# Kernel optimization log

Measured on AMD Instinct MI355X. Metric: run time of the kernel, lower is better.

## Reference

```python
import jax, jax.numpy as jnp
import numpy as np

B, T, C, DU, OUT = 16, 2048, 1024, 1024, 512
CIF_THRESHOLD = 1.0


def setup_inputs():
    key = jax.random.key(0)
    k0, k1, k2, k3, k4, k5 = jax.random.split(key, 6)
    encoder_out = jax.random.normal(k0, (B, T, C), dtype=jnp.float32)
    input_lengths = (T // 2 + jax.random.randint(k1, (B,), 0, T // 2)).astype(jnp.int32)
    target_lengths = (200 + jax.random.randint(k2, (B,), 0, 300)).astype(jnp.int32)
    s = 1.0 / np.sqrt(C)
    Wd = jax.random.uniform(k3, (DU, C), jnp.float32, -s, s)
    bd = jnp.zeros((DU,), jnp.float32)
    sp = 1.0 / np.sqrt(DU)
    Wp = jax.random.uniform(k4, (1, DU), jnp.float32, -sp, sp)
    bp = jnp.zeros((1,), jnp.float32)
    Wo = jax.random.uniform(k5, (OUT, C), jnp.float32, -s, s)
    return {"encoder_out": encoder_out, "input_lengths": input_lengths,
            "target_lengths": target_lengths, "Wd": Wd, "bd": bd,
            "Wp": Wp, "bp": bp, "Wo": Wo}


def _cif_forward(encoder_out, input_lengths, target_lengths, Wd, bd, Wp, bp, Wo):
    Bsz, Tlen, Cdim = encoder_out.shape
    pos = jnp.arange(Tlen)
    not_pad = (pos[None, :] < input_lengths[:, None]).astype(encoder_out.dtype)  # [B,T]

    # dense weight production: relu(x Wd^T + bd) -> sigmoid(. Wp^T + bp)
    h = jax.nn.relu(jnp.einsum('btc,dc->btd', encoder_out, Wd) + bd)
    weight = jax.nn.sigmoid(jnp.einsum('btd,od->bto', h, Wp)[..., 0] + bp[0])
    org_weight = weight * not_pad

    # training-time scaling so weights sum to target_lengths
    scale = target_lengths.astype(encoder_out.dtype) / (org_weight.sum(-1) + 1e-8)
    weight = org_weight * scale[:, None]

    padding_start_id = input_lengths  # = not_padding_mask.sum(-1)

    def step(carry, xs):
        acc_w, acc_s = carry                     # [B], [B,C]
        w, e, i = xs                             # [B], [B,C], scalar step idx
        fired = (acc_w + w) >= CIF_THRESHOLD     # [B]
        remained = 1.0 - acc_w
        new_w = jnp.where(fired, w - remained, w + acc_w)
        new_s = jnp.where(fired[:, None], (w - remained)[:, None] * e,
                          acc_s + w[:, None] * e)
        f_s = jnp.where(fired[:, None], acc_s + remained[:, None] * e, 0.0)
        f_s = jnp.where((i > padding_start_id)[:, None], 0.0, f_s)
        return (new_w, new_s), f_s

    init = (jnp.zeros((Bsz,), encoder_out.dtype),
            jnp.zeros((Bsz, Cdim), encoder_out.dtype))
    _, fired_states = jax.lax.scan(
        step, init,
        (weight.T, jnp.transpose(encoder_out, (1, 0, 2)), jnp.arange(Tlen)))
    fired_states = jnp.transpose(fired_states, (1, 0, 2))  # [B,T,C]

    fired_marks = jnp.abs(fired_states).sum(-1) != 0.0     # [B,T]
    # stable-compact fired frames to front; pad to T (upper bound of fired_max_length)
    order = jnp.argsort(jnp.logical_not(fired_marks).astype(jnp.int32), axis=1)
    n_fired = fired_marks.sum(-1)                           # [B]
    valid = pos[None, :] < n_fired[:, None]                 # [B,T]
    cif_outputs = jnp.take_along_axis(fired_states, order[:, :, None], axis=1)
    cif_outputs = cif_outputs * valid[:, :, None].astype(cif_outputs.dtype)

    idx = jnp.where(valid, order, 0).astype(jnp.int32)
    prev = jnp.concatenate([jnp.zeros((Bsz, 1), jnp.int32), idx[:, :-1]], axis=1)
    cif_durations = (idx - prev) * valid.astype(jnp.int32)

    base_mask = (pos[None, :] == 0).astype(jnp.int32)       # [1,0,0,...] fallback
    cif_out_padding_mask = jnp.where((n_fired > 0)[:, None],
                                     valid.astype(jnp.int32), base_mask)
    quantity_out = org_weight.sum(-1)                       # training branch
    cif_outputs = jnp.einsum('btc,oc->bto', cif_outputs, Wo)  # bias-free output proj
    return cif_outputs, cif_out_padding_mask, cif_durations, quantity_out


def reference(encoder_out, input_lengths, target_lengths, Wd, bd, Wp, bp, Wo):
    return _cif_forward(encoder_out, input_lengths, target_lengths,
                        Wd, bd, Wp, bp, Wo)
```

## Files before the change

kernel.cpp:

```cpp
#include <hip/hip_runtime.h>
#include <cstdint>
#include <cstddef>

#define BSZ 16
#define TLEN 2048
#define CDIM 1024
#define OUTDIM 512
#define MAXF 512

typedef _Float16 f16x8 __attribute__((ext_vector_type(8)));
typedef _Float16 f16x4 __attribute__((ext_vector_type(4)));
typedef float f32x16 __attribute__((ext_vector_type(16)));

__device__ __forceinline__ void gl_lds16(const void* g, void* l) {
    __builtin_amdgcn_global_load_lds(
        (const __attribute__((address_space(1))) void*)g,
        (__attribute__((address_space(3))) void*)l, 16, 0, 0);
}

struct h2pair { _Float16 h0, h1; };
__device__ __forceinline__ h2pair split2(float a) {
    h2pair o;
    o.h0 = (_Float16)a;
    float r = a - (float)o.h0;
    o.h1 = (_Float16)(r * 2048.0f);
    return o;
}

__global__ __launch_bounds__(128) void k0a_split_wd(
    const float* __restrict__ Wd, _Float16* __restrict__ B0,
    _Float16* __restrict__ B1)
{
    const int dut = blockIdx.x;
    const int ktl = blockIdx.y;
    const int r = threadIdx.x;
    const float* src = Wd + (size_t)(dut * 128 + r) * CDIM + ktl * 32;
    float v[32];
#pragma unroll
    for (int j = 0; j < 8; j++) *(float4*)&v[j * 4] = *(const float4*)(src + j * 4);
    const size_t tb = (size_t)(dut * 32 + ktl) * 4096;
#pragma unroll
    for (int c = 0; c < 4; c++) {
        f16x8 h0, h1;
#pragma unroll
        for (int j = 0; j < 8; j++) {
            h2pair s = split2(v[c * 8 + j]);
            h0[j] = s.h0;
            h1[j] = s.h1;
        }
        *(f16x8*)&B0[tb + (c * 128 + r) * 8] = h0;
        *(f16x8*)&B1[tb + (c * 128 + r) * 8] = h1;
    }
}

__global__ __launch_bounds__(256) void k0c_split_wo(
    const float* __restrict__ Wo, _Float16* __restrict__ W0,
    _Float16* __restrict__ W1)
{
    const int i = (blockIdx.x * 256 + threadIdx.x) * 4;
    float4 v = *(const float4*)(Wo + i);
    f16x4 h0, h1;
    h2pair s0 = split2(v.x); h0[0] = s0.h0; h1[0] = s0.h1;
    h2pair s1 = split2(v.y); h0[1] = s1.h0; h1[1] = s1.h1;
    h2pair s2 = split2(v.z); h0[2] = s2.h0; h1[2] = s2.h1;
    h2pair s3 = split2(v.w); h0[3] = s3.h0; h1[3] = s3.h1;
    *(f16x4*)&W0[i] = h0;
    *(f16x4*)&W1[i] = h1;
}

__global__ __launch_bounds__(512, 4) void k1_weight_gemm(
    const float* __restrict__ enc, const _Float16* __restrict__ BT0,
    const _Float16* __restrict__ BT1, const float* __restrict__ bd,
    const float* __restrict__ Wp, float* __restrict__ g)
{
    __shared__ __align__(16) _Float16 lds[32768];

    const int tid = threadIdx.x;
    const int lane = tid & 63;
    const int wv = tid >> 6;
    const int l5 = lane & 31;
    const int hi = lane >> 5;
    const int mtb = (wv & 1) * 64;
    const int ntb = (wv >> 1) * 32;

    const int bx = blockIdx.x;
    const int xcd = bx & 7;
    const int j = bx >> 3;
    const int rg = xcd * 32 + (j >> 3);
    const int dug = j & 7;
    const long row0 = (long)rg * 128;
    const int du0 = dug * 128;

    const int sgrp = wv >> 2;
    const int sq = wv & 3;
    const int sr = sgrp * 64 + lane;
    const float* aptr = enc + (row0 + sr) * (long)CDIM + sq * 8;
    const int aw0 = (sq * 128 + sr) * 8;

    const _Float16* bsrc = (sgrp ? BT1 : BT0)
        + (size_t)(dug * 32) * 4096 + sq * 1024 + lane * 8;
    const int bldofs = 8192 + sgrp * 4096 + sq * 1024;

    f32x16 acc[2], accc[2];
#pragma unroll
    for (int mt = 0; mt < 2; mt++)
#pragma unroll
        for (int r = 0; r < 16; r++) { acc[mt][r] = 0.f; accc[mt][r] = 0.f; }

    float fa[8];

    *(float4*)&fa[0] = *(const float4*)(aptr + 0);
    *(float4*)&fa[4] = *(const float4*)(aptr + 4);
    gl_lds16(bsrc, &lds[bldofs]);
    gl_lds16(bsrc + 512, &lds[bldofs + 512]);
    asm volatile("" ::: "memory");
    {
        f16x8 h0, h1;
#pragma unroll
        for (int jj = 0; jj < 8; jj++) {
            h2pair s = split2(fa[jj]);
            h0[jj] = s.h0;
            h1[jj] = s.h1;
        }
        *(f16x8*)&lds[aw0] = h0;
        *(f16x8*)&lds[4096 + aw0] = h1;
    }
    *(float4*)&fa[0] = *(const float4*)(aptr + 32);
    *(float4*)&fa[4] = *(const float4*)(aptr + 36);
    asm volatile("s_waitcnt vmcnt(2) lgkmcnt(0)" ::: "memory");
    __builtin_amdgcn_s_barrier();

    for (int kt = 0; kt < 32; ++kt) {
        const int cur = (kt & 1) * 16384;
        const int nxt = cur ^ 16384;
        __builtin_amdgcn_sched_barrier(0);

        if (kt < 31) {
            const _Float16* bs = bsrc + (size_t)(kt + 1) * 4096;
            gl_lds16(bs, &lds[nxt + bldofs]);
            gl_lds16(bs + 512, &lds[nxt + bldofs + 512]);
            asm volatile("" ::: "memory");
            f16x8 h0, h1;
#pragma unroll
            for (int jj = 0; jj < 8; jj++) {
                h2pair s = split2(fa[jj]);
                h0[jj] = s.h0;
                h1[jj] = s.h1;
            }
            *(f16x8*)&lds[nxt + aw0] = h0;
            *(f16x8*)&lds[nxt + 4096 + aw0] = h1;
            if (kt < 30) {
                *(float4*)&fa[0] = *(const float4*)(aptr + (kt + 2) * 32);
                *(float4*)&fa[4] = *(const float4*)(aptr + (kt + 2) * 32 + 4);
            }
            asm volatile("" ::: "memory");
        }

#pragma unroll
        for (int p = 0; p < 2; p++) {
            const int cq = p * 2 + hi;
            f16x8 A0[2], A1[2], B0, B1;
#pragma unroll
            for (int mt = 0; mt < 2; mt++) {
                const int ro = (cq * 128 + mtb + mt * 32 + l5) * 8;
                A0[mt] = *(const f16x8*)&lds[cur + ro];
                A1[mt] = *(const f16x8*)&lds[cur + 4096 + ro];
            }
            {
                const int ro = (cq * 128 + ntb + l5) * 8;
                B0 = *(const f16x8*)&lds[cur + 8192 + ro];
                B1 = *(const f16x8*)&lds[cur + 12288 + ro];
            }
            __builtin_amdgcn_s_setprio(1);
#pragma unroll
            for (int mt = 0; mt < 2; mt++) {
                acc[mt] = __builtin_amdgcn_mfma_f32_32x32x16_f16(
                    A0[mt], B0, acc[mt], 0, 0, 0);
                accc[mt] = __builtin_amdgcn_mfma_f32_32x32x16_f16(
                    A0[mt], B1, accc[mt], 0, 0, 0);
                accc[mt] = __builtin_amdgcn_mfma_f32_32x32x16_f16(
                    A1[mt], B0, accc[mt], 0, 0, 0);
            }
            __builtin_amdgcn_s_setprio(0);
        }

        if (kt < 31) {
            if (kt < 30)
                asm volatile("s_waitcnt vmcnt(2) lgkmcnt(0)" ::: "memory");
            else
                asm volatile("s_waitcnt vmcnt(0) lgkmcnt(0)" ::: "memory");
            __builtin_amdgcn_s_barrier();
        }
    }

    const float bdv = bd[du0 + ntb + l5];
    const float wpv = Wp[du0 + ntb + l5];
    float out = 0.f;
#pragma unroll
    for (int mt = 0; mt < 2; mt++)
#pragma unroll
        for (int r = 0; r < 16; r++) {
            float h = acc[mt][r] + 4.8828125e-4f * accc[mt][r] + bdv;
            h = h > 0.f ? h : 0.f;
            float s = wpv * h;
            s += __shfl_xor(s, 1);
            s += __shfl_xor(s, 2);
            s += __shfl_xor(s, 4);
            s += __shfl_xor(s, 8);
            s += __shfl_xor(s, 16);
            if (l5 == mt * 16 + r) out = s;
        }
    const int mt_sel = l5 >> 4;
    const int r_sel = l5 & 15;
    const int row = mtb + mt_sel * 32 + (r_sel & 3) + 8 * (r_sel >> 2) + 4 * hi;
    atomicAdd(&g[row0 + row], out);
}

__global__ __launch_bounds__(256) void k2_scan(
    const float* __restrict__ g, const int* __restrict__ in_len,
    const int* __restrict__ tgt_len, const float* __restrict__ bp,
    float* __restrict__ c_a, float* __restrict__ c_b,
    int* __restrict__ fire_t, int* __restrict__ n_fired,
    float* __restrict__ out_mask, float* __restrict__ out_dur,
    float* __restrict__ out_qty)
{
    __shared__ float w[TLEN];
    __shared__ float ca[TLEN];
    __shared__ float cb[TLEN];
    __shared__ int fires[MAXF];
    __shared__ float ssum[256];
    __shared__ float s_scale;
    __shared__ int s_nf;

    const int b = blockIdx.x;
    const int tid = threadIdx.x;
    const int len = in_len[b];
    const float bpv = bp[0];

    float local = 0.f;
    for (int t = tid; t < TLEN; t += 256) {
        float gv = g[b * TLEN + t] + bpv;
        float s = 1.f / (1.f + expf(-gv));
        float ow = (t < len) ? s : 0.f;
        w[t] = ow;
        local += ow;
    }
    ssum[tid] = local;
    __syncthreads();
    for (int st = 128; st > 0; st >>= 1) {
        if (tid < st) ssum[tid] += ssum[tid + st];
        __syncthreads();
    }
    if (tid == 0) {
        float org_sum = ssum[0];
        out_qty[b] = org_sum;
        s_scale = (float)tgt_len[b] / (org_sum + 1e-8f);
    }
    __syncthreads();
    float scale = s_scale;
    for (int t = tid; t < TLEN; t += 256) w[t] *= scale;
    __syncthreads();

    if (tid == 0) {
        float accw = 0.f;
        int k = 0;
        int t = 0;
        for (; t + 8 <= len; t += 8) {
            float4 wa = *(const float4*)&w[t];
            float4 wb4 = *(const float4*)&w[t + 4];
            float wv8[8] = {wa.x, wa.y, wa.z, wa.w, wb4.x, wb4.y, wb4.z, wb4.w};
#pragma unroll
            for (int u = 0; u < 8; u++) {
                float wt = wv8[u];
                float aw = accw + wt;
                bool f = (aw >= 1.0f);
                float rem = 1.0f - accw;
                float fb = wt - rem;
                ca[t + u] = f ? rem : wt;
                cb[t + u] = f ? fb : 0.f;
                fires[k & (MAXF - 1)] = t + u;
                k += f ? 1 : 0;
                accw = f ? fb : aw;
            }
        }
        for (; t < len; t++) {
            float wt = w[t];
            float aw = accw + wt;
            bool f = (aw >= 1.0f);
            float rem = 1.0f - accw;
            float fb = wt - rem;
            ca[t] = f ? rem : wt;
            cb[t] = f ? fb : 0.f;
            fires[k & (MAXF - 1)] = t;
            k += f ? 1 : 0;
            accw = f ? fb : aw;
        }
        s_nf = (k < MAXF) ? k : MAXF;
        n_fired[b] = s_nf;
    }
    __syncthreads();

    for (int t = tid; t < len; t += 256) {
        c_a[b * TLEN + t] = ca[t];
        c_b[b * TLEN + t] = cb[t];
    }
    const int nf = s_nf;
    for (int jj = tid; jj < nf; jj += 256) {
        int tj = fires[jj];
        fire_t[b * MAXF + jj] = tj;
        out_mask[b * TLEN + jj] = 1.0f;
        int prev = (jj == 0) ? 0 : fires[jj - 1];
        out_dur[b * TLEN + jj] = (float)(tj - prev);
    }
    if (tid == 0 && nf == 0) out_mask[b * TLEN] = 1.0f;
}

__global__ __launch_bounds__(256) void k3a_compact(
    const float* __restrict__ enc, const float* __restrict__ c_a,
    const float* __restrict__ c_b, const int* __restrict__ fire_t,
    const int* __restrict__ n_fired, _Float16* __restrict__ C0,
    _Float16* __restrict__ C1)
{
    const int b = blockIdx.y;
    const int k = blockIdx.x;
    const int tid = threadIdx.x;
    _Float16* d0 = C0 + ((size_t)b * MAXF + k) * CDIM + tid * 4;
    _Float16* d1 = C1 + ((size_t)b * MAXF + k) * CDIM + tid * 4;
    if (k >= n_fired[b]) {
        f16x4 z = {(_Float16)0.f, (_Float16)0.f, (_Float16)0.f, (_Float16)0.f};
        *(f16x4*)d0 = z;
        *(f16x4*)d1 = z;
        return;
    }
    const int tend = fire_t[b * MAXF + k];
    const int tprev = (k == 0) ? -1 : fire_t[b * MAXF + k - 1];
    float ax = 0.f, ay = 0.f, az = 0.f, aw = 0.f;
    const int tstart = (tprev < 0) ? 0 : tprev;
    for (int t = tstart; t <= tend; t++) {
        float coef = (t == tprev) ? c_b[b * TLEN + t] : c_a[b * TLEN + t];
        const float4 e = *(const float4*)(enc + ((size_t)b * TLEN + t) * CDIM + tid * 4);
        ax += coef * e.x;
        ay += coef * e.y;
        az += coef * e.z;
        aw += coef * e.w;
    }
    f16x4 h0, h1;
    h2pair s0 = split2(ax); h0[0] = s0.h0; h1[0] = s0.h1;
    h2pair s1 = split2(ay); h0[1] = s1.h0; h1[1] = s1.h1;
    h2pair s2 = split2(az); h0[2] = s2.h0; h1[2] = s2.h1;
    h2pair s3 = split2(aw); h0[3] = s3.h0; h1[3] = s3.h1;
    *(f16x4*)d0 = h0;
    *(f16x4*)d1 = h1;
}

__global__ __launch_bounds__(256, 2) void k3b_outproj(
    const _Float16* __restrict__ C0, const _Float16* __restrict__ C1,
    const _Float16* __restrict__ W0, const _Float16* __restrict__ W1,
    const int* __restrict__ n_fired, float* __restrict__ out0)
{
    __shared__ __align__(16) _Float16 lds[16384];

    const int b = blockIdx.z;
    const int nf = n_fired[b];
    const int j0 = blockIdx.x * 128;
    if (j0 >= nf) return;
    const int o0 = blockIdx.y * 128;
    const int tid = threadIdx.x;
    const int lane = tid & 63;
    const int wv = tid >> 6;
    const int l5 = lane & 31;
    const int hi = lane >> 5;
    const int mtb = (wv & 1) * 64;
    const int ntb = (wv >> 1) * 64;

    const int sr = tid >> 1;
    const int sh = tid & 1;
    const _Float16* a0p = C0 + ((size_t)b * MAXF + j0 + sr) * CDIM + sh * 16;
    const _Float16* a1p = C1 + ((size_t)b * MAXF + j0 + sr) * CDIM + sh * 16;
    const _Float16* b0p = W0 + (size_t)(o0 + sr) * CDIM + sh * 16;
    const _Float16* b1p = W1 + (size_t)(o0 + sr) * CDIM + sh * 16;

    f32x16 acc[2][2], accc[2][2];
#pragma unroll
    for (int mt = 0; mt < 2; mt++)
#pragma unroll
        for (int nt = 0; nt < 2; nt++)
#pragma unroll
            for (int r = 0; r < 16; r++) { acc[mt][nt][r] = 0.f; accc[mt][nt][r] = 0.f; }

    f16x8 xa0[2], xa1[2], xb0[2], xb1[2];
#pragma unroll
    for (int c = 0; c < 2; c++) {
        xa0[c] = *(const f16x8*)(a0p + c * 8);
        xa1[c] = *(const f16x8*)(a1p + c * 8);
        xb0[c] = *(const f16x8*)(b0p + c * 8);
        xb1[c] = *(const f16x8*)(b1p + c * 8);
    }

    for (int kt = 0; kt < 32; ++kt) {
        __syncthreads();
#pragma unroll
        for (int c = 0; c < 2; c++) {
            *(f16x8*)&lds[((sh * 2 + c) * 128 + sr) * 8] = xa0[c];
            *(f16x8*)&lds[4096 + ((sh * 2 + c) * 128 + sr) * 8] = xa1[c];
            *(f16x8*)&lds[8192 + ((sh * 2 + c) * 128 + sr) * 8] = xb0[c];
            *(f16x8*)&lds[12288 + ((sh * 2 + c) * 128 + sr) * 8] = xb1[c];
        }
        __syncthreads();
        if (kt < 31) {
            const int o = (kt + 1) * 32;
#pragma unroll
            for (int c = 0; c < 2; c++) {
                xa0[c] = *(const f16x8*)(a0p + o + c * 8);
                xa1[c] = *(const f16x8*)(a1p + o + c * 8);
                xb0[c] = *(const f16x8*)(b0p + o + c * 8);
                xb1[c] = *(const f16x8*)(b1p + o + c * 8);
            }
        }
#pragma unroll
        for (int ks = 0; ks < 2; ks++) {
            const int ch = ks * 2 + hi;
            f16x8 A0[2], A1[2], B0[2], B1[2];
#pragma unroll
            for (int mt = 0; mt < 2; mt++) {
                const int row = mtb + mt * 32 + l5;
                A0[mt] = *(const f16x8*)&lds[(ch * 128 + row) * 8];
                A1[mt] = *(const f16x8*)&lds[4096 + (ch * 128 + row) * 8];
            }
#pragma unroll
            for (int nt = 0; nt < 2; nt++) {
                const int row = ntb + nt * 32 + l5;
                B0[nt] = *(const f16x8*)&lds[8192 + (ch * 128 + row) * 8];
                B1[nt] = *(const f16x8*)&lds[12288 + (ch * 128 + row) * 8];
            }
#pragma unroll
            for (int mt = 0; mt < 2; mt++)
#pragma unroll
                for (int nt = 0; nt < 2; nt++) {
                    acc[mt][nt] = __builtin_amdgcn_mfma_f32_32x32x16_f16(
                        A0[mt], B0[nt], acc[mt][nt], 0, 0, 0);
                    accc[mt][nt] = __builtin_amdgcn_mfma_f32_32x32x16_f16(
                        A0[mt], B1[nt], accc[mt][nt], 0, 0, 0);
                    accc[mt][nt] = __builtin_amdgcn_mfma_f32_32x32x16_f16(
                        A1[mt], B0[nt], accc[mt][nt], 0, 0, 0);
                }
        }
    }

#pragma unroll
    for (int mt = 0; mt < 2; mt++)
#pragma unroll
        for (int nt = 0; nt < 2; nt++)
#pragma unroll
            for (int r = 0; r < 16; r++) {
                float val = acc[mt][nt][r] + 4.8828125e-4f * accc[mt][nt][r];
                int m = mtb + mt * 32 + (r & 3) + 8 * (r >> 2) + 4 * hi;
                int col = o0 + ntb + nt * 32 + l5;
                out0[((size_t)b * TLEN + j0 + m) * OUTDIM + col] = val;
            }
}

extern "C" void kernel_launch(void* const* d_in, const int* in_sizes, int n_in,
                              void* d_out, int out_size, void* d_ws, size_t ws_size,
                              hipStream_t stream)
{
    const float* enc = (const float*)d_in[0];
    const int* in_len = (const int*)d_in[1];
    const int* tgt_len = (const int*)d_in[2];
    const float* Wd = (const float*)d_in[3];
    const float* bd = (const float*)d_in[4];
    const float* Wp = (const float*)d_in[5];
    const float* bp = (const float*)d_in[6];
    const float* Wo = (const float*)d_in[7];

    char* ws = (char*)d_ws;
    float* g       = (float*)(ws + 0);
    float* c_a     = (float*)(ws + 131072);
    float* c_b     = (float*)(ws + 262144);
    int* fire_t    = (int*)(ws + 393216);
    int* n_fired   = (int*)(ws + 425984);
    _Float16* WdT0 = (_Float16*)(ws + 458752);
    _Float16* WdT1 = (_Float16*)(ws + 2555904);
    _Float16* Wo0  = (_Float16*)(ws + 4653056);
    _Float16* Wo1  = (_Float16*)(ws + 5701632);
    _Float16* C0   = (_Float16*)(ws + 6750208);
    _Float16* C1   = (_Float16*)(ws + 23527424);

    float* out0 = (float*)d_out;
    float* out_mask = out0 + (size_t)BSZ * TLEN * OUTDIM;
    float* out_dur = out_mask + (size_t)BSZ * TLEN;
    float* out_qty = out_dur + (size_t)BSZ * TLEN;

    (void)hipMemsetAsync(g, 0, 131072, stream);
    (void)hipMemsetAsync(d_out, 0, (size_t)out_size * 4, stream);

    k0a_split_wd<<<dim3(8, 32), 128, 0, stream>>>(Wd, WdT0, WdT1);
    k0c_split_wo<<<512, 256, 0, stream>>>(Wo, Wo0, Wo1);
    k1_weight_gemm<<<2048, 512, 0, stream>>>(enc, WdT0, WdT1, bd, Wp, g);
    k2_scan<<<BSZ, 256, 0, stream>>>(g, in_len, tgt_len, bp, c_a, c_b,
                                     fire_t, n_fired, out_mask, out_dur, out_qty);
    k3a_compact<<<dim3(MAXF, BSZ), 256, 0, stream>>>(enc, c_a, c_b, fire_t,
                                                     n_fired, C0, C1);
    k3b_outproj<<<dim3(4, 4, BSZ), 256, 0, stream>>>(C0, C1, Wo0, Wo1,
                                                     n_fired, out0);
}
```

Measured before the change: 598.3 us.

## Restructure weight GEMM to 1024-thread blocks with B operands loaded into registers

The k1 weight GEMM now runs with 16 waves per block. Each wave computes a single 32x32 output tile instead of two. The Wd split-fp16 operand is read straight from global memory into double-buffered registers rather than staged through LDS, which halves LDS use to one buffer pair for A only. The aim is more waves for latency hiding and less LDS traffic. In exchange, each wave issues more global loads, and register pressure rises under a launch-bounds request of 1024 threads with 4 blocks, which may force spills or an occupancy clamp.

```diff
diff --git a/kernel.cpp b/kernel.cpp
--- a/kernel.cpp
+++ b/kernel.cpp
@@ -68,20 +68,20 @@
     *(f16x4*)&W1[i] = h1;
 }
 
-__global__ __launch_bounds__(512, 4) void k1_weight_gemm(
+__global__ __launch_bounds__(1024, 4) void k1_weight_gemm(
     const float* __restrict__ enc, const _Float16* __restrict__ BT0,
     const _Float16* __restrict__ BT1, const float* __restrict__ bd,
     const float* __restrict__ Wp, float* __restrict__ g)
 {
-    __shared__ __align__(16) _Float16 lds[32768];
+    __shared__ __align__(16) _Float16 lds[16384];
 
     const int tid = threadIdx.x;
     const int lane = tid & 63;
     const int wv = tid >> 6;
     const int l5 = lane & 31;
     const int hi = lane >> 5;
-    const int mtb = (wv & 1) * 64;
-    const int ntb = (wv >> 1) * 32;
+    const int wm = wv & 3;
+    const int wn = wv >> 2;
 
     const int bx = blockIdx.x;
     const int xcd = bx & 7;
@@ -91,129 +91,115 @@
     const long row0 = (long)rg * 128;
     const int du0 = dug * 128;
 
-    const int sgrp = wv >> 2;
-    const int sq = wv & 3;
-    const int sr = sgrp * 64 + lane;
-    const float* aptr = enc + (row0 + sr) * (long)CDIM + sq * 8;
-    const int aw0 = (sq * 128 + sr) * 8;
-
-    const _Float16* bsrc = (sgrp ? BT1 : BT0)
-        + (size_t)(dug * 32) * 4096 + sq * 1024 + lane * 8;
-    const int bldofs = 8192 + sgrp * 4096 + sq * 1024;
-
-    f32x16 acc[2], accc[2];
-#pragma unroll
-    for (int mt = 0; mt < 2; mt++)
-#pragma unroll
-        for (int r = 0; r < 16; r++) { acc[mt][r] = 0.f; accc[mt][r] = 0.f; }
-
-    float fa[8];
-
-    *(float4*)&fa[0] = *(const float4*)(aptr + 0);
-    *(float4*)&fa[4] = *(const float4*)(aptr + 4);
-    gl_lds16(bsrc, &lds[bldofs]);
-    gl_lds16(bsrc + 512, &lds[bldofs + 512]);
-    asm volatile("" ::: "memory");
+    const int sr = tid >> 3;
+    const int sq = tid & 7;
+    const float* aptr = enc + (row0 + sr) * (long)CDIM + sq * 4;
+    const int awofs = ((sq >> 1) * 128 + sr) * 8 + (sq & 1) * 4;
+
+    const _Float16* bt0 = BT0 + (size_t)(dug * 32) * 4096
+                        + (size_t)(hi * 128 + wn * 32 + l5) * 8;
+    const _Float16* bt1 = BT1 + (size_t)(dug * 32) * 4096
+                        + (size_t)(hi * 128 + wn * 32 + l5) * 8;
+
+    f32x16 acc, accc;
+#pragma unroll
+    for (int r = 0; r < 16; r++) { acc[r] = 0.f; accc[r] = 0.f; }
+
+    float4 fa;
+    f16x8 B00, B01, B10, B11, N00, N01, N10, N11;
+
+    fa = *(const float4*)(aptr);
     {
-        f16x8 h0, h1;
-#pragma unroll
-        for (int jj = 0; jj < 8; jj++) {
-            h2pair s = split2(fa[jj]);
-            h0[jj] = s.h0;
-            h1[jj] = s.h1;
-        }
-        *(f16x8*)&lds[aw0] = h0;
-        *(f16x8*)&lds[4096 + aw0] = h1;
-    }
-    *(float4*)&fa[0] = *(const float4*)(aptr + 32);
-    *(float4*)&fa[4] = *(const float4*)(aptr + 36);
-    asm volatile("s_waitcnt vmcnt(2) lgkmcnt(0)" ::: "memory");
+        f16x4 h0, h1;
+        h2pair s0 = split2(fa.x); h0[0] = s0.h0; h1[0] = s0.h1;
+        h2pair s1 = split2(fa.y); h0[1] = s1.h0; h1[1] = s1.h1;
+        h2pair s2 = split2(fa.z); h0[2] = s2.h0; h1[2] = s2.h1;
+        h2pair s3 = split2(fa.w); h0[3] = s3.h0; h1[3] = s3.h1;
+        *(f16x4*)&lds[awofs] = h0;
+        *(f16x4*)&lds[4096 + awofs] = h1;
+    }
+    B00 = *(const f16x8*)(bt0);
+    B01 = *(const f16x8*)(bt0 + 2048);
+    B10 = *(const f16x8*)(bt1);
+    B11 = *(const f16x8*)(bt1 + 2048);
+    fa = *(const float4*)(aptr + 32);
+    asm volatile("s_waitcnt lgkmcnt(0)" ::: "memory");
     __builtin_amdgcn_s_barrier();
 
-    for (int kt = 0; kt < 32; ++kt) {
-        const int cur = (kt & 1) * 16384;
-        const int nxt = cur ^ 16384;
-        __builtin_amdgcn_sched_barrier(0);
-
-        if (kt < 31) {
-            const _Float16* bs = bsrc + (size_t)(kt + 1) * 4096;
-            gl_lds16(bs, &lds[nxt + bldofs]);
-            gl_lds16(bs + 512, &lds[nxt + bldofs + 512]);
-            asm volatile("" ::: "memory");
-            f16x8 h0, h1;
-#pragma unroll
-            for (int jj = 0; jj < 8; jj++) {
-                h2pair s = split2(fa[jj]);
-                h0[jj] = s.h0;
-                h1[jj] = s.h1;
-            }
-            *(f16x8*)&lds[nxt + aw0] = h0;
-            *(f16x8*)&lds[nxt + 4096 + aw0] = h1;
-            if (kt < 30) {
-                *(float4*)&fa[0] = *(const float4*)(aptr + (kt + 2) * 32);
-                *(float4*)&fa[4] = *(const float4*)(aptr + (kt + 2) * 32 + 4);
-            }
-            asm volatile("" ::: "memory");
-        }
-
-#pragma unroll
-        for (int p = 0; p < 2; p++) {
-            const int cq = p * 2 + hi;
-            f16x8 A0[2], A1[2], B0, B1;
-#pragma unroll
-            for (int mt = 0; mt < 2; mt++) {
-                const int ro = (cq * 128 + mtb + mt * 32 + l5) * 8;
-                A0[mt] = *(const f16x8*)&lds[cur + ro];
-                A1[mt] = *(const f16x8*)&lds[cur + 4096 + ro];
-            }
-            {
-                const int ro = (cq * 128 + ntb + l5) * 8;
-                B0 = *(const f16x8*)&lds[cur + 8192 + ro];
-                B1 = *(const f16x8*)&lds[cur + 12288 + ro];
-            }
-            __builtin_amdgcn_s_setprio(1);
-#pragma unroll
-            for (int mt = 0; mt < 2; mt++) {
-                acc[mt] = __builtin_amdgcn_mfma_f32_32x32x16_f16(
-                    A0[mt], B0, acc[mt], 0, 0, 0);
-                accc[mt] = __builtin_amdgcn_mfma_f32_32x32x16_f16(
-                    A0[mt], B1, accc[mt], 0, 0, 0);
-                accc[mt] = __builtin_amdgcn_mfma_f32_32x32x16_f16(
-                    A1[mt], B0, accc[mt], 0, 0, 0);
-            }
-            __builtin_amdgcn_s_setprio(0);
-        }
-
-        if (kt < 31) {
-            if (kt < 30)
-                asm volatile("s_waitcnt vmcnt(2) lgkmcnt(0)" ::: "memory");
-            else
-                asm volatile("s_waitcnt vmcnt(0) lgkmcnt(0)" ::: "memory");
-            __builtin_amdgcn_s_barrier();
-        }
-    }
-
-    const float bdv = bd[du0 + ntb + l5];
-    const float wpv = Wp[du0 + ntb + l5];
+#define K1_STEP(KT, BC00, BC01, BC10, BC11, BN00, BN01, BN10, BN11)            \
+    {                                                                          \
+        const int kt_ = (KT);                                                  \
+        const int cur = (kt_ & 1) * 8192;                                      \
+        const int nxt = cur ^ 8192;                                            \
+        if (kt_ < 31) {                                                        \
+            const _Float16* b0_ = bt0 + (size_t)(kt_ + 1) * 4096;              \
+            const _Float16* b1_ = bt1 + (size_t)(kt_ + 1) * 4096;              \
+            BN00 = *(const f16x8*)(b0_);                                       \
+            BN01 = *(const f16x8*)(b0_ + 2048);                                \
+            BN10 = *(const f16x8*)(b1_);                                       \
+            BN11 = *(const f16x8*)(b1_ + 2048);                                \
+        }                                                                      \
+        asm volatile("" ::: "memory");                                         \
+        if (kt_ < 31) {                                                        \
+            f16x4 h0_, h1_;                                                    \
+            h2pair s0_ = split2(fa.x); h0_[0] = s0_.h0; h1_[0] = s0_.h1;       \
+            h2pair s1_ = split2(fa.y); h0_[1] = s1_.h0; h1_[1] = s1_.h1;       \
+            h2pair s2_ = split2(fa.z); h0_[2] = s2_.h0; h1_[2] = s2_.h1;       \
+            h2pair s3_ = split2(fa.w); h0_[3] = s3_.h0; h1_[3] = s3_.h1;       \
+            *(f16x4*)&lds[nxt + awofs] = h0_;                                  \
+            *(f16x4*)&lds[nxt + 4096 + awofs] = h1_;                           \
+            if (kt_ < 30)                                                      \
+                fa = *(const float4*)(aptr + (kt_ + 2) * 32);                  \
+        }                                                                      \
+        asm volatile("" ::: "memory");                                         \
+        f16x8 A00, A10, A01, A11;                                              \
+        {                                                                      \
+            const int ro0 = ((0 * 2 + hi) * 128 + wm * 32 + l5) * 8;           \
+            const int ro1 = ((1 * 2 + hi) * 128 + wm * 32 + l5) * 8;           \
+            A00 = *(const f16x8*)&lds[cur + ro0];                              \
+            A10 = *(const f16x8*)&lds[cur + 4096 + ro0];                       \
+            A01 = *(const f16x8*)&lds[cur + ro1];                              \
+            A11 = *(const f16x8*)&lds[cur + 4096 + ro1];                       \
+        }                                                                      \
+        __builtin_amdgcn_s_setprio(1);                                         \
+        acc  = __builtin_amdgcn_mfma_f32_32x32x16_f16(A00, BC00, acc, 0, 0, 0);\
+        accc = __builtin_amdgcn_mfma_f32_32x32x16_f16(A00, BC10, accc, 0, 0, 0);\
+        accc = __builtin_amdgcn_mfma_f32_32x32x16_f16(A10, BC00, accc, 0, 0, 0);\
+        acc  = __builtin_amdgcn_mfma_f32_32x32x16_f16(A01, BC01, acc, 0, 0, 0);\
+        accc = __builtin_amdgcn_mfma_f32_32x32x16_f16(A01, BC11, accc, 0, 0, 0);\
+        accc = __builtin_amdgcn_mfma_f32_32x32x16_f16(A11, BC01, accc, 0, 0, 0);\
+        __builtin_amdgcn_s_setprio(0);                                         \
+        if (kt_ < 31) {                                                        \
+            asm volatile("s_waitcnt lgkmcnt(0)" ::: "memory");                 \
+            __builtin_amdgcn_s_barrier();                                      \
+        }                                                                      \
+    }
+
+    for (int k2 = 0; k2 < 16; k2++) {
+        K1_STEP(2 * k2,     B00, B01, B10, B11, N00, N01, N10, N11);
+        K1_STEP(2 * k2 + 1, N00, N01, N10, N11, B00, B01, B10, B11);
+    }
+#undef K1_STEP
+
+    const float bdv = bd[du0 + wn * 32 + l5];
+    const float wpv = Wp[du0 + wn * 32 + l5];
     float out = 0.f;
 #pragma unroll
-    for (int mt = 0; mt < 2; mt++)
-#pragma unroll
-        for (int r = 0; r < 16; r++) {
-            float h = acc[mt][r] + 4.8828125e-4f * accc[mt][r] + bdv;
-            h = h > 0.f ? h : 0.f;
-            float s = wpv * h;
-            s += __shfl_xor(s, 1);
-            s += __shfl_xor(s, 2);
-            s += __shfl_xor(s, 4);
-            s += __shfl_xor(s, 8);
-            s += __shfl_xor(s, 16);
-            if (l5 == mt * 16 + r) out = s;
-        }
-    const int mt_sel = l5 >> 4;
-    const int r_sel = l5 & 15;
-    const int row = mtb + mt_sel * 32 + (r_sel & 3) + 8 * (r_sel >> 2) + 4 * hi;
-    atomicAdd(&g[row0 + row], out);
+    for (int r = 0; r < 16; r++) {
+        float h = acc[r] + 4.8828125e-4f * accc[r] + bdv;
+        h = h > 0.f ? h : 0.f;
+        float s = wpv * h;
+        s += __shfl_xor(s, 1);
+        s += __shfl_xor(s, 2);
+        s += __shfl_xor(s, 4);
+        s += __shfl_xor(s, 8);
+        s += __shfl_xor(s, 16);
+        if (l5 == r) out = s;
+    }
+    if (l5 < 16) {
+        const int row = wm * 32 + (l5 & 3) + 8 * (l5 >> 2) + 4 * hi;
+        atomicAdd(&g[row0 + row], out);
+    }
 }
 
 __global__ __launch_bounds__(256) void k2_scan(
@@ -496,7 +482,7 @@
 
     k0a_split_wd<<<dim3(8, 32), 128, 0, stream>>>(Wd, WdT0, WdT1);
     k0c_split_wo<<<512, 256, 0, stream>>>(Wo, Wo0, Wo1);
-    k1_weight_gemm<<<2048, 512, 0, stream>>>(enc, WdT0, WdT1, bd, Wp, g);
+    k1_weight_gemm<<<2048, 1024, 0, stream>>>(enc, WdT0, WdT1, bd, Wp, g);
     k2_scan<<<BSZ, 256, 0, stream>>>(g, in_len, tgt_len, bp, c_a, c_b,
                                      fire_t, n_fired, out_mask, out_dur, out_qty);
     k3a_compact<<<dim3(MAXF, BSZ), 256, 0, stream>>>(enc, c_a, c_b, fire_t,
```

Result: slower. 703.1 us (+17.5%).
